# Kernel optimization log

Measured on AMD Instinct MI355X. Metric: run time of the kernel, lower is better.

The kernel has to match this reference:

```python
import jax, jax.numpy as jnp
import numpy as np

DT = 0.01
DX = 1.0
DY = 1.0
NUM_STEPS = 10


def _diff(a, axis, h):
    """Central difference in the interior, one-sided at boundaries, along `axis`.
    a: [B, H, W]; returns same shape."""
    def sl(s):
        idx = [slice(None)] * a.ndim
        idx[axis] = s
        return a[tuple(idx)]
    left = (sl(slice(1, 2)) - sl(slice(0, 1))) / h            # one-sided forward at boundary 0
    interior = (sl(slice(2, None)) - sl(slice(None, -2))) / (2.0 * h)
    right = (sl(slice(-1, None)) - sl(slice(-2, -1))) / h     # one-sided backward at boundary -1
    return jnp.concatenate([left, interior, right], axis=axis)


def _diffusion_step(u, alpha, beta, aniso_x, aniso_y):
    # u: [B, H, W]; axis 1 = y, axis 2 = x (matches torch indexing)
    grad_x = _diff(u, axis=2, h=DX)
    grad_y = _diff(u, axis=1, h=DY)
    flux_x = (alpha * aniso_x) * grad_x   # scalars broadcast
    flux_y = (beta * aniso_y) * grad_y
    div_flux = _diff(flux_x, axis=2, h=DX) + _diff(flux_y, axis=1, h=DY)
    return u + DT * div_flux


def setup_inputs() -> dict:
    key = jax.random.key(0)
    k1, = jax.random.split(key, 1)
    u = jax.random.normal(k1, (64, 1, 512, 512), dtype=jnp.float32)
    ones = jnp.ones((1,), dtype=jnp.float32)
    return {
        "u": u,
        "alpha": ones * 0.5,
        "beta": ones * 0.5,
        "aniso_x": ones,
        "aniso_y": ones,
        "edge_strength": ones * 0.1,
    }


def reference(u, alpha, beta, aniso_x, aniso_y, edge_strength):
    # u: [B, 1, H, W] -> squeeze channel
    x = u[:, 0]                       # [B, H, W]
    x_orig = x

    def body(carry, _):
        return _diffusion_step(carry, alpha, beta, aniso_x, aniso_y), None

    x, _ = jax.lax.scan(body, x, None, length=NUM_STEPS)
    alpha_mix = jax.nn.sigmoid(edge_strength)   # shape (1,), broadcasts
    out = alpha_mix * x + (1.0 - alpha_mix) * x_orig
    return out[:, None]               # [B, 1, H, W]
```

## Files before the change

kernel.cpp:

```cpp
#include <hip/hip_runtime.h>
#include <math.h>

#define W 512
#define H 512
#define IMG (W * H)
#define LSTRIDE 84
#define LWORDS 6400

__host__ __device__ constexpr double dcoefd(int i, int j) {
    if (i == 0) return j == 0 ? 0.5 : j == 1 ? -1.0 : j == 2 ? 0.5 : 0.0;
    if (i == 1) return j == 0 ? 0.5 : j == 1 ? -0.75 : j == 3 ? 0.25 : 0.0;
    return j == i - 2 ? 0.25 : j == i ? -0.5 : j == i + 2 ? 0.25 : 0.0;
}

struct GhostT {
    float g[7][8];
    constexpr GhostT() : g{} {
        double v0[8] = {}, v1[8] = {}, v2[8] = {}, w0[8] = {}, w1r[8] = {}, w2r[8] = {};
        for (int j = 0; j < 8; ++j) { v0[j] = dcoefd(0, j); v1[j] = dcoefd(1, j); v2[j] = dcoefd(2, j); }
        for (int j = 0; j < 8; ++j) {
            double s0 = 0, s1 = 0, s2 = 0;
            for (int k = 0; k < 10; ++k) {
                s0 += dcoefd(0, k) * dcoefd(k, j);
                s1 += dcoefd(1, k) * dcoefd(k, j);
                s2 += dcoefd(2, k) * dcoefd(k, j);
            }
            w0[j] = s0; w1r[j] = s1; w2r[j] = s2;
        }
        double um1[8] = {}, um2[8] = {}, um3[8] = {}, um4[8] = {}, um5[8] = {}, um6[8] = {};
        double vm1[8] = {}, vm2[8] = {}, vm3[8] = {}, vm4[8] = {}, wm1[8] = {}, wm2[8] = {};
        for (int j = 0; j < 8; ++j) {
            um1[j] = 2.0 * (j == 0) - (j == 1);
            um2[j] = 4.0 * (j == 0) - 4.0 * (j == 1) + (j == 2);
            vm1[j] = 2 * v0[j] - v1[j];
            vm2[j] = 4 * v0[j] - 4 * v1[j] + v2[j];
            wm1[j] = 2 * w0[j] - w1r[j];
            wm2[j] = 4 * w0[j] - 4 * w1r[j] + w2r[j];
        }
        for (int j = 0; j < 8; ++j) {
            um3[j] = 4 * vm1[j] + 2 * um1[j] - (j == 1);
            um4[j] = 4 * vm2[j] + 2 * um2[j] - (j == 0);
            vm3[j] = 4 * wm1[j] + 2 * vm1[j] - v1[j];
            vm4[j] = 4 * wm2[j] + 2 * vm2[j] - v0[j];
        }
        for (int j = 0; j < 8; ++j) {
            um5[j] = 4 * vm3[j] + 2 * um3[j] - um1[j];
            um6[j] = 4 * vm4[j] + 2 * um4[j] - um2[j];
        }
        for (int j = 0; j < 8; ++j) {
            g[1][j] = (float)um1[j]; g[2][j] = (float)um2[j]; g[3][j] = (float)um3[j];
            g[4][j] = (float)um4[j]; g[5][j] = (float)um5[j]; g[6][j] = (float)um6[j];
        }
    }
};
constexpr GhostT GH{};

__device__ __forceinline__ float4 ld4(const float* p) {
    return *reinterpret_cast<const float4*>(p);
}
__device__ __forceinline__ float rfl(float x) {
    return __int_as_float(__builtin_amdgcn_readfirstlane(__float_as_int(x)));
}

struct Uni {
    float k1, k2, k3, m1, m2, n1;
    float wy1a, wy1b, wy2a, wy2b, wy2c, wy3a, wy3b, wy3c, wy3d;
    float am, iam;
};

template<int CLS, int RI>
__device__ __forceinline__ void row_lds(const Uni& U, const float* __restrict__ lbase,
                                        float acc[4][4]) {
    const float* rowp = lbase + 2 * RI * LSTRIDE;
    float u0a[4], t1a[4], t2a[4], t3a[4];
    if (CLS == 0) {
        const float4 m2 = ld4(rowp + 8);
        u0a[0] = m2.x; u0a[1] = m2.y; u0a[2] = m2.z; u0a[3] = m2.w;
    } else if (CLS <= 2) {
        const float4 m1 = ld4(rowp + 4);
        const float4 m2 = ld4(rowp + 8);
        const float4 m3 = ld4(rowp + 12);
        u0a[0] = m2.x; u0a[1] = m2.y; u0a[2] = m2.z; u0a[3] = m2.w;
        t1a[0] = m1.z + m2.z; t1a[1] = m1.w + m2.w;
        t1a[2] = m2.x + m3.x; t1a[3] = m2.y + m3.y;
        t2a[0] = m1.x + m3.x; t2a[1] = m1.y + m3.y;
        t2a[2] = m1.z + m3.z; t2a[3] = m1.w + m3.w;
    } else {
        const float4 m0 = ld4(rowp);
        const float4 m4 = ld4(rowp + 16);
        const float4 m1 = ld4(rowp + 4);
        const float4 m3 = ld4(rowp + 12);
        t3a[0] = m0.z + m3.z; t3a[1] = m0.w + m3.w;
        t3a[2] = m1.x + m4.x; t3a[3] = m1.y + m4.y;
        t2a[0] = m1.x + m3.x; t2a[1] = m1.y + m3.y;
        t2a[2] = m1.z + m3.z; t2a[3] = m1.w + m3.w;
        const float4 m2 = ld4(rowp + 8);
        t1a[0] = m1.z + m2.z; t1a[1] = m1.w + m2.w;
        t1a[2] = m2.x + m3.x; t1a[3] = m2.y + m3.y;
        u0a[0] = m2.x; u0a[1] = m2.y; u0a[2] = m2.z; u0a[3] = m2.w;
    }

    #pragma unroll
    for (int j = 0; j < 4; ++j) {
        const float u0 = u0a[j];
        const float M3v = 120.f * u0;
        float M2v = 0.f, M1v = 0.f, M0v = 0.f;
        if (CLS >= 1) {
            const float X1 = fmaf(0.25f, t1a[j], -0.5f * u0);
            M2v = fmaf(U.n1, X1, 45.f * u0);
            if (CLS >= 2) {
                const float X2 = fmaf(0.0625f, t2a[j], fmaf(-0.25f, t1a[j], 0.375f * u0));
                M1v = fmaf(U.m1, X1, fmaf(U.m2, X2, 10.f * u0));
                if (CLS >= 3) {
                    const float X3 = fmaf(1.f/64, t3a[j], fmaf(-6.f/64, t2a[j],
                                      fmaf(15.f/64, t1a[j], (-20.f/64) * u0)));
                    M0v = fmaf(U.k1, X1, fmaf(U.k2, X2, U.k3 * X3));
                }
            }
        }
        #pragma unroll
        for (int k = 0; k < 4; ++k) {
            const int dq = RI - 3 - k;
            const int ad = dq < 0 ? -dq : dq;
            if (ad > 3) continue;
            float a = acc[k][j];
            if (ad == 0) {
                a = fmaf(U.iam, u0, a);
                a += M0v;
                a = fmaf(U.wy1b, M1v, a);
                a = fmaf(U.wy2c, M2v, a);
                a = fmaf(U.wy3d, M3v, a);
            } else if (ad == 1) {
                a = fmaf(U.wy1a, M1v, a);
                a = fmaf(U.wy2b, M2v, a);
                a = fmaf(U.wy3c, M3v, a);
            } else if (ad == 2) {
                a = fmaf(U.wy2a, M2v, a);
                a = fmaf(U.wy3b, M3v, a);
            } else {
                a = fmaf(U.wy3a, M3v, a);
            }
            acc[k][j] = a;
        }
    }
}

__global__ __launch_bounds__(256, 8) void fused_v14(
        const float* __restrict__ uin, float* __restrict__ outp,
        const float* __restrict__ alpha, const float* __restrict__ beta,
        const float* __restrict__ axp, const float* __restrict__ ayp,
        const float* __restrict__ es) {
    __shared__ float lds0[LWORDS];

    const unsigned bid = blockIdx.x;
    const unsigned swz = (bid & 7u) * (gridDim.x >> 3) + (bid >> 3);
    const unsigned img  = swz >> 6;
    const unsigned tile = swz & 63u;
    const int gx0 = (int)(tile & 7u) << 6;
    const int gy0 = (int)(tile >> 3) << 6;
    const float* __restrict__ p = uin + (size_t)img * IMG;
    float* __restrict__ q = outp + (size_t)img * IMG;

    const int tid = threadIdx.x;
    const int wid = tid >> 6, lane = tid & 63;

    for (int t = wid; t < 25; t += 4) {
        int idx = (t << 8) + (lane << 2);
        int row = (int)((unsigned)idx / 84u);
        if (row > 75) row = 75;
        int col = idx - row * 84;
        int gy = gy0 + row - 6;
        gy = gy < 0 ? 0 : (gy > H - 1 ? H - 1 : gy);
        int gx = gx0 + col - 8;
        gx = gx < 0 ? 0 : (gx > W - 4 ? W - 4 : gx);
        const float* src = p + (size_t)gy * W + gx;
        __builtin_amdgcn_global_load_lds(
            (const __attribute__((address_space(1))) void*)src,
            (__attribute__((address_space(3))) void*)&lds0[t << 8],
            16, 0, 0);
    }
    __syncthreads();

    if (gy0 == 0 || gy0 == H - 64) {
        if (tid < 20) {
            const int w0 = tid << 2;
            #pragma unroll
            for (int k = 1; k <= 6; ++k) {
                float4 a = {0.f, 0.f, 0.f, 0.f};
                #pragma unroll
                for (int j = 0; j < 8; ++j) {
                    const float w = GH.g[k][j];
                    if (w != 0.f) {
                        const int srow = (gy0 == 0) ? (6 + j) : (69 - j);
                        const float4 r = ld4(&lds0[srow * LSTRIDE + w0]);
                        a.x = fmaf(w, r.x, a.x); a.y = fmaf(w, r.y, a.y);
                        a.z = fmaf(w, r.z, a.z); a.w = fmaf(w, r.w, a.w);
                    }
                }
                const int drow = (gy0 == 0) ? (6 - k) : (69 + k);
                *reinterpret_cast<float4*>(&lds0[drow * LSTRIDE + w0]) = a;
            }
        }
        __syncthreads();
    }

    if (gx0 == 0 || gx0 == W - 64) {
        if (tid < 76) {
            float* rp = &lds0[tid * LSTRIDE];
            #pragma unroll
            for (int k = 1; k <= 6; ++k) {
                float s = 0.f;
                #pragma unroll
                for (int j = 0; j < 8; ++j) {
                    const float w = GH.g[k][j];
                    if (w != 0.f) {
                        const float v = (gx0 == 0) ? rp[8 + j] : rp[71 - j];
                        s = fmaf(w, v, s);
                    }
                }
                if (gx0 == 0) rp[8 - k] = s; else rp[71 + k] = s;
            }
        }
        __syncthreads();
    }

    const float sx = 0.01f * alpha[0] * axp[0];
    const float sy = 0.01f * beta[0]  * ayp[0];
    Uni U;
    U.k1 = rfl(10.f * sx);  U.k2 = rfl(45.f * sx * sx);  U.k3 = rfl(120.f * sx * sx * sx);
    U.m1 = rfl(90.f * sx);  U.m2 = rfl(360.f * sx * sx); U.n1 = rfl(360.f * sx);
    const float sy2 = sy * sy, sy3 = sy2 * sy;
    U.wy1a = rfl(0.25f * sy);    U.wy1b = rfl(-0.5f * sy);
    U.wy2a = rfl(0.0625f * sy2); U.wy2b = rfl(-0.25f * sy2); U.wy2c = rfl(0.375f * sy2);
    U.wy3a = rfl((1.f/64) * sy3);  U.wy3b = rfl((-6.f/64) * sy3);
    U.wy3c = rfl((15.f/64) * sy3); U.wy3d = rfl((-20.f/64) * sy3);
    const float amv = 1.f / (1.f + expf(-es[0]));
    U.am = rfl(amv); U.iam = rfl(1.f / amv);

    const int qc = tid & 15, g = tid >> 4;
    const int y0 = ((g >> 1) << 3) + (g & 1);
    const int x0 = qc << 2;
    const float* lbase = &lds0[y0 * LSTRIDE + x0];

    float acc[4][4] = {};
    row_lds<0, 0>(U, lbase, acc);
    row_lds<1, 1>(U, lbase, acc);
    row_lds<2, 2>(U, lbase, acc);
    row_lds<3, 3>(U, lbase, acc);
    row_lds<3, 4>(U, lbase, acc);
    row_lds<3, 5>(U, lbase, acc);
    row_lds<3, 6>(U, lbase, acc);
    row_lds<2, 7>(U, lbase, acc);
    row_lds<1, 8>(U, lbase, acc);
    row_lds<0, 9>(U, lbase, acc);

    #pragma unroll
    for (int k = 0; k < 4; ++k) {
        const int Yo = gy0 + y0 + 2 * k;
        float4 o;
        o.x = U.am * acc[k][0];
        o.y = U.am * acc[k][1];
        o.z = U.am * acc[k][2];
        o.w = U.am * acc[k][3];
        *reinterpret_cast<float4*>(q + (size_t)Yo * W + gx0 + x0) = o;
    }
}

extern "C" void kernel_launch(void* const* d_in, const int* in_sizes, int n_in,
                              void* d_out, int out_size, void* d_ws, size_t ws_size,
                              hipStream_t stream) {
    const float* u     = (const float*)d_in[0];
    const float* alpha = (const float*)d_in[1];
    const float* beta  = (const float*)d_in[2];
    const float* ax    = (const float*)d_in[3];
    const float* ay    = (const float*)d_in[4];
    const float* es    = (const float*)d_in[5];
    float* out = (float*)d_out;

    int nimg = in_sizes[0] / IMG;
    dim3 block(256);
    dim3 grid((unsigned)(nimg * 64));
    fused_v14<<<grid, block, 0, stream>>>(u, out, alpha, beta, ax, ay, es);
}
```

Measured before the change: 34.41 us.

## Give each wavefront a private halo slab to remove block-wide barriers

Each of the four wavefronts now loads its own 28-row halo slab of the tile into a private LDS region and waits only on its own vector-memory counter instead of a block barrier. Boundary ghost-row and ghost-column fills are done per wave on its own slab, so all __syncthreads calls are gone. The cost is redundant halo loads (4×28 rows instead of 76) and more LDS per block, and the min-blocks launch bound is dropped, which may change occupancy.

```diff
diff --git a/kernel.cpp b/kernel.cpp
--- a/kernel.cpp
+++ b/kernel.cpp
@@ -5,7 +5,8 @@
 #define H 512
 #define IMG (W * H)
 #define LSTRIDE 84
-#define LWORDS 6400
+#define WWORDS 2560
+#define LWORDS (4 * WWORDS)
 
 __host__ __device__ constexpr double dcoefd(int i, int j) {
     if (i == 0) return j == 0 ? 0.5 : j == 1 ? -1.0 : j == 2 ? 0.5 : 0.0;
@@ -145,7 +146,7 @@
     }
 }
 
-__global__ __launch_bounds__(256, 8) void fused_v14(
+__global__ __launch_bounds__(256) void fused_v17(
         const float* __restrict__ uin, float* __restrict__ outp,
         const float* __restrict__ alpha, const float* __restrict__ beta,
         const float* __restrict__ axp, const float* __restrict__ ayp,
@@ -163,65 +164,76 @@
 
     const int tid = threadIdx.x;
     const int wid = tid >> 6, lane = tid & 63;
-
-    for (int t = wid; t < 25; t += 4) {
+    const int WB = wid * WWORDS;
+    const int wrow0 = 16 * wid - 6;
+
+    #pragma unroll
+    for (int t = 0; t < 10; ++t) {
         int idx = (t << 8) + (lane << 2);
-        int row = (int)((unsigned)idx / 84u);
-        if (row > 75) row = 75;
-        int col = idx - row * 84;
-        int gy = gy0 + row - 6;
+        int lr  = (int)((unsigned)idx / 84u);
+        int col = idx - lr * 84;
+        int gy = gy0 + wrow0 + lr;
         gy = gy < 0 ? 0 : (gy > H - 1 ? H - 1 : gy);
         int gx = gx0 + col - 8;
         gx = gx < 0 ? 0 : (gx > W - 4 ? W - 4 : gx);
         const float* src = p + (size_t)gy * W + gx;
         __builtin_amdgcn_global_load_lds(
             (const __attribute__((address_space(1))) void*)src,
-            (__attribute__((address_space(3))) void*)&lds0[t << 8],
+            (__attribute__((address_space(3))) void*)&lds0[WB + idx],
             16, 0, 0);
     }
-    __syncthreads();
-
-    if (gy0 == 0 || gy0 == H - 64) {
-        if (tid < 20) {
-            const int w0 = tid << 2;
+    asm volatile("s_waitcnt vmcnt(0)" ::: "memory");
+
+    if (gy0 == 0 && wid == 0 && lane < 20) {
+        const int w0 = lane << 2;
+        #pragma unroll
+        for (int k = 1; k <= 6; ++k) {
+            float4 a = {0.f, 0.f, 0.f, 0.f};
             #pragma unroll
-            for (int k = 1; k <= 6; ++k) {
-                float4 a = {0.f, 0.f, 0.f, 0.f};
-                #pragma unroll
-                for (int j = 0; j < 8; ++j) {
-                    const float w = GH.g[k][j];
-                    if (w != 0.f) {
-                        const int srow = (gy0 == 0) ? (6 + j) : (69 - j);
-                        const float4 r = ld4(&lds0[srow * LSTRIDE + w0]);
-                        a.x = fmaf(w, r.x, a.x); a.y = fmaf(w, r.y, a.y);
-                        a.z = fmaf(w, r.z, a.z); a.w = fmaf(w, r.w, a.w);
-                    }
-                }
-                const int drow = (gy0 == 0) ? (6 - k) : (69 + k);
-                *reinterpret_cast<float4*>(&lds0[drow * LSTRIDE + w0]) = a;
-            }
-        }
-        __syncthreads();
-    }
-
-    if (gx0 == 0 || gx0 == W - 64) {
-        if (tid < 76) {
-            float* rp = &lds0[tid * LSTRIDE];
+            for (int j = 0; j < 8; ++j) {
+                const float w = GH.g[k][j];
+                if (w != 0.f) {
+                    const float4 r = ld4(&lds0[WB + (6 + j) * LSTRIDE + w0]);
+                    a.x = fmaf(w, r.x, a.x); a.y = fmaf(w, r.y, a.y);
+                    a.z = fmaf(w, r.z, a.z); a.w = fmaf(w, r.w, a.w);
+                }
+            }
+            *reinterpret_cast<float4*>(&lds0[WB + (6 - k) * LSTRIDE + w0]) = a;
+        }
+    }
+    if (gy0 == H - 64 && wid == 3 && lane < 20) {
+        const int w0 = lane << 2;
+        #pragma unroll
+        for (int k = 1; k <= 6; ++k) {
+            float4 a = {0.f, 0.f, 0.f, 0.f};
             #pragma unroll
-            for (int k = 1; k <= 6; ++k) {
-                float s = 0.f;
-                #pragma unroll
-                for (int j = 0; j < 8; ++j) {
-                    const float w = GH.g[k][j];
-                    if (w != 0.f) {
-                        const float v = (gx0 == 0) ? rp[8 + j] : rp[71 - j];
-                        s = fmaf(w, v, s);
-                    }
-                }
-                if (gx0 == 0) rp[8 - k] = s; else rp[71 + k] = s;
-            }
-        }
-        __syncthreads();
+            for (int j = 0; j < 8; ++j) {
+                const float w = GH.g[k][j];
+                if (w != 0.f) {
+                    const float4 r = ld4(&lds0[WB + (21 - j) * LSTRIDE + w0]);
+                    a.x = fmaf(w, r.x, a.x); a.y = fmaf(w, r.y, a.y);
+                    a.z = fmaf(w, r.z, a.z); a.w = fmaf(w, r.w, a.w);
+                }
+            }
+            *reinterpret_cast<float4*>(&lds0[WB + (21 + k) * LSTRIDE + w0]) = a;
+        }
+    }
+
+    if ((gx0 == 0 || gx0 == W - 64) && lane < 28) {
+        float* rp = &lds0[WB + lane * LSTRIDE];
+        #pragma unroll
+        for (int k = 1; k <= 6; ++k) {
+            float s = 0.f;
+            #pragma unroll
+            for (int j = 0; j < 8; ++j) {
+                const float w = GH.g[k][j];
+                if (w != 0.f) {
+                    const float v = (gx0 == 0) ? rp[8 + j] : rp[71 - j];
+                    s = fmaf(w, v, s);
+                }
+            }
+            if (gx0 == 0) rp[8 - k] = s; else rp[71 + k] = s;
+        }
     }
 
     const float sx = 0.01f * alpha[0] * axp[0];
@@ -237,10 +249,11 @@
     const float amv = 1.f / (1.f + expf(-es[0]));
     U.am = rfl(amv); U.iam = rfl(1.f / amv);
 
-    const int qc = tid & 15, g = tid >> 4;
-    const int y0 = ((g >> 1) << 3) + (g & 1);
+    const int qc = tid & 15;
+    const int gw = (tid >> 4) & 3;
+    const int ly0 = ((gw >> 1) << 3) + (gw & 1);
     const int x0 = qc << 2;
-    const float* lbase = &lds0[y0 * LSTRIDE + x0];
+    const float* lbase = &lds0[WB + ly0 * LSTRIDE + x0];
 
     float acc[4][4] = {};
     row_lds<0, 0>(U, lbase, acc);
@@ -254,9 +267,10 @@
     row_lds<1, 8>(U, lbase, acc);
     row_lds<0, 9>(U, lbase, acc);
 
+    const int ybase = gy0 + 16 * wid + ly0;
     #pragma unroll
     for (int k = 0; k < 4; ++k) {
-        const int Yo = gy0 + y0 + 2 * k;
+        const int Yo = ybase + 2 * k;
         float4 o;
         o.x = U.am * acc[k][0];
         o.y = U.am * acc[k][1];
@@ -280,5 +294,5 @@
     int nimg = in_sizes[0] / IMG;
     dim3 block(256);
     dim3 grid((unsigned)(nimg * 64));
-    fused_v14<<<grid, block, 0, stream>>>(u, out, alpha, beta, ax, ay, es);
-}
+    fused_v17<<<grid, block, 0, stream>>>(u, out, alpha, beta, ax, ay, es);
+}
```

Result: no change. 34.13 us (-0.8%).
